# Performance work log

Measured on AMD Instinct MI355X. Metric: run time of the kernel, lower is better.

## Reference

```python
import jax, jax.numpy as jnp
import numpy as np

NUM_JOINTS = 24
IN_DIM = 256      # PoseMLP hidden_dim (per-joint input feature)
HID = 128         # MLP default hidden_dim
OUT_DIM = 6
B = 16384

def setup_inputs() -> dict:
    key = jax.random.key(0)
    ks = jax.random.split(key, 7)
    s1 = 1.0 / np.sqrt(IN_DIM)   # torch Linear init scale (uniform bound)
    s2 = 1.0 / np.sqrt(HID)
    return {
        "pose_feat": jax.random.normal(ks[0], (B, NUM_JOINTS, IN_DIM), dtype=jnp.float32),
        # stacked per-joint weights: Linear stores W as (out, in); we keep (in, out)
        "W1": jax.random.uniform(ks[1], (NUM_JOINTS, IN_DIM, HID), minval=-s1, maxval=s1, dtype=jnp.float32),
        "b1": jax.random.uniform(ks[2], (NUM_JOINTS, HID), minval=-s1, maxval=s1, dtype=jnp.float32),
        "W2": jax.random.uniform(ks[3], (NUM_JOINTS, HID, HID), minval=-s2, maxval=s2, dtype=jnp.float32),
        "b2": jax.random.uniform(ks[4], (NUM_JOINTS, HID), minval=-s2, maxval=s2, dtype=jnp.float32),
        "W3": jax.random.uniform(ks[5], (NUM_JOINTS, HID, OUT_DIM), minval=-s2, maxval=s2, dtype=jnp.float32),
        "b3": jax.random.uniform(ks[6], (NUM_JOINTS, OUT_DIM), minval=-s2, maxval=s2, dtype=jnp.float32),
    }

def reference(pose_feat, W1, b1, W2, b2, W3, b3):
    # Batched per-joint MLPs (fuses the 24 independent small MLPs into 3 grouped GEMMs)
    h = jax.nn.relu(jnp.einsum('bji,jih->bjh', pose_feat, W1) + b1)  # [B,24,128]
    h = jax.nn.relu(jnp.einsum('bjh,jhk->bjk', h, W2) + b2)          # [B,24,128]
    out = jnp.einsum('bjh,jho->bjo', h, W3) + b3                     # [B,24,6]
    return out
```

## Files before the change

kernel.cpp:

```cpp
#include <hip/hip_runtime.h>
#include <hip/hip_fp16.h>

typedef _Float16 half_t;
typedef __attribute__((ext_vector_type(8))) _Float16 half8;
typedef __attribute__((ext_vector_type(4))) _Float16 half4;
typedef __attribute__((ext_vector_type(4))) float floatx4;

#define NJ 24
#define IN_DIM 256
#define HID 128
#define OUT_DIM 6
#define BATCH 16384
#define BM 128

#define W1_JSTRIDE (8 * 128 * 32)
#define W2_JSTRIDE (4 * 128 * 32)
#define W3_JSTRIDE (16 * 128)
#define WT1_ELEMS (NJ * W1_JSTRIDE)
#define WT2_ELEMS (NJ * W2_JSTRIDE)
#define WT3_ELEMS (NJ * W3_JSTRIDE)
#define WT2_OFF WT1_ELEMS
#define WT3_OFF (WT1_ELEMS + WT2_ELEMS)
#define B3P_BYTE_OFF ((size_t)(WT1_ELEMS + WT2_ELEMS + WT3_ELEMS) * 2)
#define PREP_TOTAL (WT1_ELEMS + WT2_ELEMS + WT3_ELEMS + NJ * 16)

__global__ void posemlp_prep(const float* __restrict__ W1, const float* __restrict__ W2,
                             const float* __restrict__ W3, const float* __restrict__ b3,
                             half_t* __restrict__ wt, float* __restrict__ b3p) {
    int t = blockIdx.x * 256 + threadIdx.x;
    if (t < WT1_ELEMS) {
        int j = t / W1_JSTRIDE, r = t % W1_JSTRIDE;
        int ks = r / 4096, r2 = r % 4096;
        int n = r2 / 32, kk = r2 % 32, k = ks * 32 + kk;
        wt[t] = (half_t)W1[((size_t)j * IN_DIM + k) * HID + n];
    } else if (t < WT2_OFF + WT2_ELEMS) {
        int u = t - WT2_OFF;
        int j = u / W2_JSTRIDE, r = u % W2_JSTRIDE;
        int ks = r / 4096, r2 = r % 4096;
        int n = r2 / 32, kk = r2 % 32, k = ks * 32 + kk;
        wt[t] = (half_t)W2[((size_t)j * HID + k) * HID + n];
    } else if (t < WT3_OFF + WT3_ELEMS) {
        int u = t - WT3_OFF;
        int j = u / W3_JSTRIDE, r = u % W3_JSTRIDE;
        int n = r / 128, k = r % 128;
        wt[t] = (n < OUT_DIM) ? (half_t)W3[((size_t)j * HID + k) * OUT_DIM + n] : (half_t)0.0f;
    } else if (t < PREP_TOTAL) {
        int u = t - WT3_OFF - WT3_ELEMS;
        int j = u / 16, n = u % 16;
        b3p[u] = (n < OUT_DIM) ? b3[j * OUT_DIM + n] : 0.0f;
    }
}

__device__ inline void gll16(const void* g, void* l) {
    __builtin_amdgcn_global_load_lds(
        (const __attribute__((address_space(1))) unsigned int*)g,
        (__attribute__((address_space(3))) unsigned int*)l, 16, 0, 0);
}

#define VMWAIT(N) asm volatile("s_waitcnt vmcnt(" #N ")" ::: "memory")
#define LGKM0()                                     \
    do {                                            \
        asm volatile("s_waitcnt lgkmcnt(0)" ::: "memory"); \
        __builtin_amdgcn_sched_barrier(0);          \
    } while (0)
__device__ inline void barrier_pinned() {
    __builtin_amdgcn_sched_barrier(0);
    __builtin_amdgcn_s_barrier();
    __builtin_amdgcn_sched_barrier(0);
}

__device__ inline half8 lds_read8(const half_t* lds, int r, int k) {
    int byte = r * 256 + k * 2;
    byte ^= (r & 7) << 4;
    return *(const half8*)((const char*)lds + byte);
}
__device__ inline void lds_write4(half_t* lds, int r, int n, half4 v) {
    int byte = r * 256 + n * 2;
    byte ^= (r & 7) << 4;
    *(half4*)((char*)lds + byte) = v;
}

__device__ inline half8 cvt8(floatx4 a, floatx4 b) {
    half8 h;
    h[0] = (_Float16)a[0]; h[1] = (_Float16)a[1]; h[2] = (_Float16)a[2]; h[3] = (_Float16)a[3];
    h[4] = (_Float16)b[0]; h[5] = (_Float16)b[1]; h[6] = (_Float16)b[2]; h[7] = (_Float16)b[3];
    return h;
}

__global__ __launch_bounds__(512, 4) void posemlp_main(
    const float* __restrict__ X, const half_t* __restrict__ wt,
    const float* __restrict__ b1, const float* __restrict__ b2,
    const float* __restrict__ b3p, float* __restrict__ out) {
    __shared__ half_t wbuf[2][4096];
    __shared__ half_t w3buf[2048];
    __shared__ half_t h_lds[BM * HID];

    const int bid = blockIdx.x;
    const int j = bid >> 7;
    const int row0 = (bid & 127) * BM;
    const int tid = threadIdx.x;
    const int w = tid >> 6;
    const int l = tid & 63;
    const int lrow = l & 15;
    const int q = l >> 4;
    const int myrow = w * 16 + lrow;

    const float* xq = X + ((size_t)(row0 + myrow) * NJ + j) * IN_DIM + q * 8;

    const half_t* w1j = wt + (size_t)j * W1_JSTRIDE;
    const half_t* w2j = wt + WT2_OFF + (size_t)j * W2_JSTRIDE;
    const half_t* w3j = wt + WT3_OFF + (size_t)j * W3_JSTRIDE;

    const int sn = tid >> 2, ss = tid & 3;
    const int wsrc_off = sn * 32 + (ss ^ ((sn >> 1) & 3)) * 8;
    half_t* wdst0 = &wbuf[0][w * 512];
    half_t* wdst1 = &wbuf[1][w * 512];

    floatx4 px[2][2];
    px[0][0] = *(const floatx4*)(xq);
    px[0][1] = *(const floatx4*)(xq + 4);
    gll16(w1j + wsrc_off, wdst0);
    if (tid < 256) {
        const int tn = tid >> 4, ts = tid & 15;
        gll16(w3j + tn * 128 + (ts ^ tn) * 8, &w3buf[w * 512]);
    }
    gll16(w1j + 4096 + wsrc_off, wdst1);

    floatx4 acc[8] = {};
#pragma unroll
    for (int ks = 0; ks < 8; ++ks) {
        VMWAIT(1);
        barrier_pinned();
        if (ks < 7) {
            px[(ks + 1) & 1][0] = *(const floatx4*)(xq + (ks + 1) * 32);
            px[(ks + 1) & 1][1] = *(const floatx4*)(xq + (ks + 1) * 32 + 4);
        }
        half8 bx = cvt8(px[ks & 1][0], px[ks & 1][1]);
        const half_t* wb = wbuf[ks & 1];
#pragma unroll
        for (int nf = 0; nf < 8; ++nf) {
            const int n = nf * 16 + lrow;
            half8 a = *(const half8*)&wb[n * 32 + (q ^ ((n >> 1) & 3)) * 8];
            acc[nf] = __builtin_amdgcn_mfma_f32_16x16x32_f16(a, bx, acc[nf], 0, 0, 0);
        }
        LGKM0();
        barrier_pinned();
        if (ks <= 5)      gll16(w1j + (ks + 2) * 4096 + wsrc_off, (ks & 1) ? wdst1 : wdst0);
        else if (ks == 6) gll16(w2j + wsrc_off, wdst0);
        else              gll16(w2j + 4096 + wsrc_off, wdst1);
    }
    {
        const float* b1j = b1 + j * HID;
#pragma unroll
        for (int nf = 0; nf < 8; ++nf) {
            floatx4 bb = *(const floatx4*)(b1j + nf * 16 + q * 4);
            floatx4 v = acc[nf];
            half4 hv;
#pragma unroll
            for (int i = 0; i < 4; ++i) hv[i] = (_Float16)fmaxf(v[i] + bb[i], 0.0f);
            lds_write4(h_lds, myrow, nf * 16 + q * 4, hv);
        }
        LGKM0();
    }

    floatx4 acc2[8] = {};
#pragma unroll
    for (int ks = 0; ks < 4; ++ks) {
        if (ks == 3) { VMWAIT(0); } else { VMWAIT(1); }
        barrier_pinned();
        half8 bh = lds_read8(h_lds, myrow, ks * 32 + q * 8);
        const half_t* wb = wbuf[ks & 1];
#pragma unroll
        for (int nf = 0; nf < 8; ++nf) {
            const int n = nf * 16 + lrow;
            half8 a = *(const half8*)&wb[n * 32 + (q ^ ((n >> 1) & 3)) * 8];
            acc2[nf] = __builtin_amdgcn_mfma_f32_16x16x32_f16(a, bh, acc2[nf], 0, 0, 0);
        }
        LGKM0();
        barrier_pinned();
        if (ks < 2) gll16(w2j + (ks + 2) * 4096 + wsrc_off, (ks & 1) ? wdst1 : wdst0);
    }
    {
        const float* b2j = b2 + j * HID;
#pragma unroll
        for (int nf = 0; nf < 8; ++nf) {
            floatx4 bb = *(const floatx4*)(b2j + nf * 16 + q * 4);
            floatx4 v = acc2[nf];
            half4 hv;
#pragma unroll
            for (int i = 0; i < 4; ++i) hv[i] = (_Float16)fmaxf(v[i] + bb[i], 0.0f);
            lds_write4(h_lds, myrow, nf * 16 + q * 4, hv);
        }
        LGKM0();
    }

    floatx4 acc3 = {};
#pragma unroll
    for (int ks = 0; ks < 4; ++ks) {
        const int u = ks * 4 + q;
        half8 a3 = *(const half8*)&w3buf[lrow * 128 + (u ^ lrow) * 8];
        half8 bh = lds_read8(h_lds, myrow, ks * 32 + q * 8);
        acc3 = __builtin_amdgcn_mfma_f32_16x16x32_f16(a3, bh, acc3, 0, 0, 0);
    }
    {
        floatx4 bb = *(const floatx4*)(b3p + j * 16 + q * 4);
        const int orow = row0 + myrow;
        float* op = out + ((size_t)orow * NJ + j) * OUT_DIM;
        floatx4 v = acc3;
        if (q == 0) {
            float2 s0 = {v[0] + bb[0], v[1] + bb[1]};
            float2 s1 = {v[2] + bb[2], v[3] + bb[3]};
            *(float2*)(op + 0) = s0;
            *(float2*)(op + 2) = s1;
        } else if (q == 1) {
            float2 s = {v[0] + bb[0], v[1] + bb[1]};
            *(float2*)(op + 4) = s;
        }
    }
}

extern "C" void kernel_launch(void* const* d_in, const int* in_sizes, int n_in,
                              void* d_out, int out_size, void* d_ws, size_t ws_size,
                              hipStream_t stream) {
    const float* X  = (const float*)d_in[0];
    const float* W1 = (const float*)d_in[1];
    const float* b1 = (const float*)d_in[2];
    const float* W2 = (const float*)d_in[3];
    const float* b2 = (const float*)d_in[4];
    const float* W3 = (const float*)d_in[5];
    const float* b3 = (const float*)d_in[6];
    float* out = (float*)d_out;

    half_t* wt = (half_t*)d_ws;
    float* b3p = (float*)((char*)d_ws + B3P_BYTE_OFF);

    int prep_blocks = (PREP_TOTAL + 255) / 256;
    posemlp_prep<<<prep_blocks, 256, 0, stream>>>(W1, W2, W3, b3, wt, b3p);

    int grid = NJ * (BATCH / BM);
    posemlp_main<<<grid, 512, 0, stream>>>(X, wt, b1, b2, b3p, out);
}
```

Baseline: 122.9 us.

## Halve row tile, bulk-load weight slices, swizzle block order, deepen X prefetch

Shrinks the row tile from 128 to 64 and blocks from 512 to 256 threads. The double-buffered per-k-slice weight pipeline, with its manual waitcnt and barriers, is replaced by bulk loads of half a weight matrix into a larger LDS buffer, separated by a few __syncthreads. The block index is remapped so neighbouring launched blocks handle different joints and row chunks, and X loads are prefetched three k-slices ahead instead of one. The aim is more resident blocks and more memory parallelism on the X stream, at the cost of twice as many weight reloads and exposed load latency at each bulk-load barrier.

Result: slower. 132.1 us (+7.5%).

```diff
diff --git a/kernel.cpp b/kernel.cpp
--- a/kernel.cpp
+++ b/kernel.cpp
@@ -11,7 +11,7 @@
 #define HID 128
 #define OUT_DIM 6
 #define BATCH 16384
-#define BM 128
+#define BM 64
 
 #define W1_JSTRIDE (8 * 128 * 32)
 #define W2_JSTRIDE (4 * 128 * 32)
@@ -57,18 +57,6 @@
         (__attribute__((address_space(3))) unsigned int*)l, 16, 0, 0);
 }
 
-#define VMWAIT(N) asm volatile("s_waitcnt vmcnt(" #N ")" ::: "memory")
-#define LGKM0()                                     \
-    do {                                            \
-        asm volatile("s_waitcnt lgkmcnt(0)" ::: "memory"); \
-        __builtin_amdgcn_sched_barrier(0);          \
-    } while (0)
-__device__ inline void barrier_pinned() {
-    __builtin_amdgcn_sched_barrier(0);
-    __builtin_amdgcn_s_barrier();
-    __builtin_amdgcn_sched_barrier(0);
-}
-
 __device__ inline half8 lds_read8(const half_t* lds, int r, int k) {
     int byte = r * 256 + k * 2;
     byte ^= (r & 7) << 4;
@@ -87,17 +75,18 @@
     return h;
 }
 
-__global__ __launch_bounds__(512, 4) void posemlp_main(
+__global__ __launch_bounds__(256, 3) void posemlp_main(
     const float* __restrict__ X, const half_t* __restrict__ wt,
     const float* __restrict__ b1, const float* __restrict__ b2,
     const float* __restrict__ b3p, float* __restrict__ out) {
-    __shared__ half_t wbuf[2][4096];
+    __shared__ half_t wbuf[16384];
     __shared__ half_t w3buf[2048];
     __shared__ half_t h_lds[BM * HID];
 
-    const int bid = blockIdx.x;
-    const int j = bid >> 7;
-    const int row0 = (bid & 127) * BM;
+    const int bid0 = blockIdx.x;
+    const int bid = (bid0 & 7) * 768 + (bid0 >> 3);
+    const int j = bid >> 8;
+    const int row0 = (bid & 255) * BM;
     const int tid = threadIdx.x;
     const int w = tid >> 6;
     const int l = tid & 63;
@@ -112,43 +101,49 @@
     const half_t* w3j = wt + WT3_OFF + (size_t)j * W3_JSTRIDE;
 
     const int sn = tid >> 2, ss = tid & 3;
-    const int wsrc_off = sn * 32 + (ss ^ ((sn >> 1) & 3)) * 8;
-    half_t* wdst0 = &wbuf[0][w * 512];
-    half_t* wdst1 = &wbuf[1][w * 512];
-
-    floatx4 px[2][2];
+    const int wsrc = sn * 32 + (ss ^ ((sn >> 1) & 3)) * 8;
+
+    floatx4 px[3][2];
     px[0][0] = *(const floatx4*)(xq);
     px[0][1] = *(const floatx4*)(xq + 4);
-    gll16(w1j + wsrc_off, wdst0);
-    if (tid < 256) {
-        const int tn = tid >> 4, ts = tid & 15;
-        gll16(w3j + tn * 128 + (ts ^ tn) * 8, &w3buf[w * 512]);
-    }
-    gll16(w1j + 4096 + wsrc_off, wdst1);
+    px[1][0] = *(const floatx4*)(xq + 32);
+    px[1][1] = *(const floatx4*)(xq + 36);
+    px[2][0] = *(const floatx4*)(xq + 64);
+    px[2][1] = *(const floatx4*)(xq + 68);
+    {
+        const int tn = tid >> 4, tsl = tid & 15;
+        gll16(w3j + tn * 128 + (tsl ^ tn) * 8, &w3buf[w * 512]);
+    }
+#pragma unroll
+    for (int r = 0; r < 8; ++r)
+        gll16(w1j + r * 2048 + wsrc, &wbuf[r * 2048 + w * 512]);
+    __syncthreads();
+
+#define L1_ITER(ks, wbbase) do {                                            \
+        half8 bx = cvt8(px[(ks) % 3][0], px[(ks) % 3][1]);                  \
+        if ((ks) < 5) {                                                     \
+            px[(ks) % 3][0] = *(const floatx4*)(xq + ((ks) + 3) * 32);      \
+            px[(ks) % 3][1] = *(const floatx4*)(xq + ((ks) + 3) * 32 + 4);  \
+        }                                                                   \
+        _Pragma("unroll")                                                   \
+        for (int nf = 0; nf < 8; ++nf) {                                    \
+            const int n = nf * 16 + lrow;                                   \
+            half8 a = *(const half8*)&(wbbase)[n * 32 + (q ^ ((n >> 1) & 3)) * 8]; \
+            acc[nf] = __builtin_amdgcn_mfma_f32_16x16x32_f16(a, bx, acc[nf], 0, 0, 0); \
+        }                                                                   \
+    } while (0)
 
     floatx4 acc[8] = {};
 #pragma unroll
-    for (int ks = 0; ks < 8; ++ks) {
-        VMWAIT(1);
-        barrier_pinned();
-        if (ks < 7) {
-            px[(ks + 1) & 1][0] = *(const floatx4*)(xq + (ks + 1) * 32);
-            px[(ks + 1) & 1][1] = *(const floatx4*)(xq + (ks + 1) * 32 + 4);
-        }
-        half8 bx = cvt8(px[ks & 1][0], px[ks & 1][1]);
-        const half_t* wb = wbuf[ks & 1];
-#pragma unroll
-        for (int nf = 0; nf < 8; ++nf) {
-            const int n = nf * 16 + lrow;
-            half8 a = *(const half8*)&wb[n * 32 + (q ^ ((n >> 1) & 3)) * 8];
-            acc[nf] = __builtin_amdgcn_mfma_f32_16x16x32_f16(a, bx, acc[nf], 0, 0, 0);
-        }
-        LGKM0();
-        barrier_pinned();
-        if (ks <= 5)      gll16(w1j + (ks + 2) * 4096 + wsrc_off, (ks & 1) ? wdst1 : wdst0);
-        else if (ks == 6) gll16(w2j + wsrc_off, wdst0);
-        else              gll16(w2j + 4096 + wsrc_off, wdst1);
-    }
+    for (int ks = 0; ks < 4; ++ks) L1_ITER(ks, wbuf + ks * 4096);
+    __syncthreads();
+#pragma unroll
+    for (int r = 0; r < 8; ++r)
+        gll16(w1j + 16384 + r * 2048 + wsrc, &wbuf[r * 2048 + w * 512]);
+    __syncthreads();
+
+#pragma unroll
+    for (int ks = 4; ks < 8; ++ks) L1_ITER(ks, wbuf + (ks - 4) * 4096);
     {
         const float* b1j = b1 + j * HID;
 #pragma unroll
@@ -160,25 +155,23 @@
             for (int i = 0; i < 4; ++i) hv[i] = (_Float16)fmaxf(v[i] + bb[i], 0.0f);
             lds_write4(h_lds, myrow, nf * 16 + q * 4, hv);
         }
-        LGKM0();
-    }
+    }
+    __syncthreads();
+#pragma unroll
+    for (int r = 0; r < 8; ++r)
+        gll16(w2j + r * 2048 + wsrc, &wbuf[r * 2048 + w * 512]);
+    __syncthreads();
 
     floatx4 acc2[8] = {};
 #pragma unroll
     for (int ks = 0; ks < 4; ++ks) {
-        if (ks == 3) { VMWAIT(0); } else { VMWAIT(1); }
-        barrier_pinned();
         half8 bh = lds_read8(h_lds, myrow, ks * 32 + q * 8);
-        const half_t* wb = wbuf[ks & 1];
 #pragma unroll
         for (int nf = 0; nf < 8; ++nf) {
             const int n = nf * 16 + lrow;
-            half8 a = *(const half8*)&wb[n * 32 + (q ^ ((n >> 1) & 3)) * 8];
+            half8 a = *(const half8*)&wbuf[ks * 4096 + n * 32 + (q ^ ((n >> 1) & 3)) * 8];
             acc2[nf] = __builtin_amdgcn_mfma_f32_16x16x32_f16(a, bh, acc2[nf], 0, 0, 0);
         }
-        LGKM0();
-        barrier_pinned();
-        if (ks < 2) gll16(w2j + (ks + 2) * 4096 + wsrc_off, (ks & 1) ? wdst1 : wdst0);
     }
     {
         const float* b2j = b2 + j * HID;
@@ -191,7 +184,6 @@
             for (int i = 0; i < 4; ++i) hv[i] = (_Float16)fmaxf(v[i] + bb[i], 0.0f);
             lds_write4(h_lds, myrow, nf * 16 + q * 4, hv);
         }
-        LGKM0();
     }
 
     floatx4 acc3 = {};
@@ -238,5 +230,5 @@
     posemlp_prep<<<prep_blocks, 256, 0, stream>>>(W1, W2, W3, b3, wt, b3p);
 
     int grid = NJ * (BATCH / BM);
-    posemlp_main<<<grid, 512, 0, stream>>>(X, wt, b1, b2, b3p, out);
-}
+    posemlp_main<<<grid, 256, 0, stream>>>(X, wt, b1, b2, b3p, out);
+}
```
